# Optimization experiments

Measured on AMD Instinct MI355X. Metric: run time of the kernel, lower is better.

The kernel has to match this reference:

```python
import jax, jax.numpy as jnp
import numpy as np

B, C, H, W = 4, 64, 96, 96
KS, NH = 7, 4


def setup_inputs() -> dict:
    key = jax.random.key(0)
    ks = jax.random.split(key, 9)
    s = 0.1  # keep logits in a sane range for softmax
    return {
        "input_x": jax.random.normal(ks[0], (B, C, H, W), jnp.float32),
        "q_w": jax.random.normal(ks[1], (C, C), jnp.float32) * s,
        "q_b": jax.random.normal(ks[2], (C,), jnp.float32) * s,
        "k_w": jax.random.normal(ks[3], (C, C), jnp.float32) * s,
        "k_b": jax.random.normal(ks[4], (C,), jnp.float32) * s,
        "v_w": jax.random.normal(ks[5], (C, C), jnp.float32) * s,
        "v_b": jax.random.normal(ks[6], (C,), jnp.float32) * s,
        "rel_h": jax.random.normal(ks[7], (C // 2, KS, 1), jnp.float32) * s,
        "rel_w": jax.random.normal(ks[8], (C // 2, 1, KS), jnp.float32) * s,
    }


def _unfold(x, ks):
    # x: (B, C, Hp, Wp) -> (B, C, Ho, Wo, ks, ks), same as torch .unfold(2).unfold(3)
    Hp, Wp = x.shape[2], x.shape[3]
    Ho, Wo = Hp - ks + 1, Wp - ks + 1
    ih = jnp.arange(Ho)[:, None] + jnp.arange(ks)[None, :]  # (Ho, ks)
    iw = jnp.arange(Wo)[:, None] + jnp.arange(ks)[None, :]  # (Wo, ks)
    return x[:, :, ih[:, None, :, None], iw[None, :, None, :]]


def reference(input_x, q_w, q_b, k_w, k_b, v_w, v_b, rel_h, rel_w):
    b, c, h, w = input_x.shape
    ks, nh = KS, NH
    dkh = c // nh
    p0 = (ks - 1) // 2
    p1 = ks - 1 - p0
    padded = jnp.pad(input_x, ((0, 0), (0, 0), (p0, p1), (p0, p1)))

    conv1x1 = lambda x, wt, bi: jnp.einsum('bchw,oc->bohw', x, wt) + bi[None, :, None, None]
    k = conv1x1(padded, k_w, k_b)
    v = conv1x1(padded, v_w, v_b)
    q = conv1x1(input_x, q_w, q_b)

    # flat reshapes exactly as in torch (row-major), reproducing its layout semantics
    k = _unfold(k, ks).reshape(b, nh, h, w, dkh, ks * ks)
    v = _unfold(v, ks).reshape(b, nh, h, w, dkh, ks * ks)
    q = q.reshape(b, nh, h, w, dkh)  # torch: (b,nh,h,w,dkh,1) squeezed

    qk = jnp.einsum('bnxyd,bnxydk->bnxyk', q, k).reshape(b, nh, h, w, ks, ks)
    # torch einsum 'bhxydz,cij->bhxyij' == (sum_d q) outer (sum_c rel)
    qsum = q.sum(-1)  # (b, nh, h, w)
    rel = rel_h.sum(0) + rel_w.sum(0)  # broadcasts to (ks, ks)
    qk = qk + qsum[..., None, None] * rel

    weights = jax.nn.softmax(qk.reshape(b, nh, h, w, ks * ks), axis=-1)
    attn = jnp.einsum('bnxyk,bnxydk->bnxyd', weights, v)  # (b, nh, h, w, dkh)
    attn = attn.reshape(b, c, h, w)  # flat reshape, matching torch
    return jax.nn.relu(attn)
```

## Files before the change

### kernel.cpp

```cpp
#include <hip/hip_runtime.h>

#define B_ 4
#define C_ 64
#define H_ 96
#define W_ 96
#define KS_ 7
#define NPIX (H_ * W_)
#define PR_ 102
#define PC_ 104
#define PSLAB (PR_ * PC_)

typedef __attribute__((ext_vector_type(8))) short short8;
typedef __attribute__((ext_vector_type(8))) unsigned short ushort8;
typedef __attribute__((ext_vector_type(4))) float f32x4;

static __device__ inline ushort f2bf(float f) {
    union { float f; unsigned u; } v; v.f = f;
    unsigned r = (v.u + 0x7fff + ((v.u >> 16) & 1)) >> 16;
    return (ushort)r;
}
static __device__ inline float bf2f(ushort u) {
    union { unsigned u; float f; } v; v.u = ((unsigned)u) << 16; return v.f;
}


__global__ __launch_bounds__(256) void mfma_conv_kernel(
    const float* __restrict__ in,
    const float* __restrict__ qw, const float* __restrict__ qb,
    const float* __restrict__ kw, const float* __restrict__ kb,
    const float* __restrict__ vw, const float* __restrict__ vb,
    const float* __restrict__ relh, const float* __restrict__ relw,
    float* __restrict__ qf, ushort* __restrict__ kvb, float* __restrict__ rel_out)
{
    const int b    = blockIdx.y;
    const int pix0 = blockIdx.x * 32;
    const int t    = threadIdx.x;
    const int lane = t & 63;
    const int wv   = t >> 6;

    if (blockIdx.x == 0 && b == 0 && t < 49) {
        const int i = t / KS_, j = t % KS_;
        float s = 0.f;
        #pragma unroll
        for (int cc = 0; cc < C_ / 2; ++cc)
            s += relh[cc * KS_ + i] + relw[cc * KS_ + j];
        rel_out[t] = s;
    }

    {
        const int base = blockIdx.x * 256 + t;
        #pragma unroll
        for (int rep = 0; rep < 3; ++rep) {
            const int idx = base + rep * 73728;
            if (idx < 153600) {
                const int cell   = idx % 1200;
                const int chh    = (idx / 1200) & 63;
                const int tensor = idx / 76800;
                int pr, pw;
                if (cell < 312)      { pr = cell / PC_;              pw = cell % PC_; }
                else if (cell < 624) { int j2 = cell - 312; pr = 99 + j2 / PC_; pw = j2 % PC_; }
                else                 { int j2 = cell - 624; pr = 3 + j2 / 6; int s2 = j2 % 6;
                                       pw = (s2 < 3) ? s2 : 96 + s2; }
                const float bias = (tensor ? vb : kb)[chh];
                kvb[((size_t)(b * 2 + tensor) * C_ + chh) * PSLAB + pr * PC_ + pw] = f2bf(bias);
            }
        }
    }

    __shared__ ushort xs[32 * 64];

    {
        const int pix = t & 31, cg = t >> 5;
        const float* xp = in + (size_t)b * C_ * NPIX + pix0 + pix;
        #pragma unroll
        for (int g = 0; g < 2; ++g) {
            const int ch = (cg + 8 * g) * 4;
            float x0 = xp[(size_t)(ch    ) * NPIX];
            float x1 = xp[(size_t)(ch + 1) * NPIX];
            float x2 = xp[(size_t)(ch + 2) * NPIX];
            float x3 = xp[(size_t)(ch + 3) * NPIX];
            ushort4 u = make_ushort4(f2bf(x0), f2bf(x1), f2bf(x2), f2bf(x3));
            unsigned byte = (unsigned)(pix * 128 + ch * 2) ^ (unsigned)((pix & 7) << 4);
            *reinterpret_cast<ushort4*>(reinterpret_cast<char*>(xs) + byte) = u;
        }
    }

    short8 afr[3][2];
    float  bi[3][4];
    #pragma unroll
    for (int i = 0; i < 3; ++i) {
        const int mt  = 3 * wv + i;
        const int row = mt * 16 + (lane & 15);
        const float* wsrc = (mt < 4) ? qw + row * 64
                          : (mt < 8) ? kw + (row - 64) * 64
                                     : vw + (row - 128) * 64;
        #pragma unroll
        for (int ka = 0; ka < 2; ++ka) {
            const int kk = ka * 32 + (lane >> 4) * 8;
            float4 a = *reinterpret_cast<const float4*>(wsrc + kk);
            float4 c = *reinterpret_cast<const float4*>(wsrc + kk + 4);
            short8 s;
            s[0] = (short)f2bf(a.x); s[1] = (short)f2bf(a.y);
            s[2] = (short)f2bf(a.z); s[3] = (short)f2bf(a.w);
            s[4] = (short)f2bf(c.x); s[5] = (short)f2bf(c.y);
            s[6] = (short)f2bf(c.z); s[7] = (short)f2bf(c.w);
            afr[i][ka] = s;
        }
        const int brow = mt * 16 + (lane >> 4) * 4;
        const float* bsrc = (mt < 4) ? qb + brow
                          : (mt < 8) ? kb + (brow - 64)
                                     : vb + (brow - 128);
        #pragma unroll
        for (int r = 0; r < 4; ++r) bi[i][r] = bsrc[r];
    }
    __syncthreads();

    short8 bfr[2][2];
    #pragma unroll
    for (int nt = 0; nt < 2; ++nt) {
        const int pl = nt * 16 + (lane & 15);
        #pragma unroll
        for (int ka = 0; ka < 2; ++ka) {
            const int kk = ka * 32 + (lane >> 4) * 8;
            unsigned byte = (unsigned)(pl * 128 + kk * 2) ^ (unsigned)((pl & 7) << 4);
            bfr[nt][ka] = *reinterpret_cast<const short8*>(
                reinterpret_cast<const char*>(xs) + byte);
        }
    }
    f32x4 acc[3][2];
    #pragma unroll
    for (int i = 0; i < 3; ++i) {
        f32x4 bv;
        #pragma unroll
        for (int r = 0; r < 4; ++r) bv[r] = bi[i][r];
        #pragma unroll
        for (int nt = 0; nt < 2; ++nt) acc[i][nt] = bv;
    }
    #pragma unroll
    for (int i = 0; i < 3; ++i) {
        #pragma unroll
        for (int nt = 0; nt < 2; ++nt) {
            acc[i][nt] = __builtin_amdgcn_mfma_f32_16x16x32_bf16(
                afr[i][0], bfr[nt][0], acc[i][nt], 0, 0, 0);
            acc[i][nt] = __builtin_amdgcn_mfma_f32_16x16x32_bf16(
                afr[i][1], bfr[nt][1], acc[i][nt], 0, 0, 0);
        }
    }
    #pragma unroll
    for (int i = 0; i < 3; ++i) {
        const int mt = 3 * wv + i;
        #pragma unroll
        for (int nt = 0; nt < 2; ++nt) {
            const int pix = pix0 + nt * 16 + (lane & 15);
            const int h = pix / 96, w = pix - h * 96;
            #pragma unroll
            for (int r = 0; r < 4; ++r) {
                const int row = mt * 16 + (lane >> 4) * 4 + r;
                if (mt < 4) {
                    qf[((size_t)b * C_ + row) * NPIX + pix] = acc[i][nt][r];
                } else {
                    const int tensor = (mt < 8) ? 0 : 1;
                    const int ch = (mt & 3) * 16 + (lane >> 4) * 4 + r;
                    kvb[((size_t)(b * 2 + tensor) * C_ + ch) * PSLAB
                        + (h + 3) * PC_ + (w + 3)] = f2bf(acc[i][nt][r]);
                }
            }
        }
    }
}

__global__ __launch_bounds__(384) void attn_kernel(
    const float* __restrict__ qf, const ushort* __restrict__ kvb,
    const float* __restrict__ rel, float* __restrict__ out)
{
    const int bx   = blockIdx.x;
    const int tile = bx % 3;
    const int c    = (bx / 3) % C_;
    const int b    = bx / (3 * C_);
    const int ho0  = tile * 32;
    const int t    = threadIdx.x;

    __shared__ __align__(16) ushort kvls[2][38 * PC_];

    {
        const ushort* kbase = kvb + ((size_t)(b * 2 + 0) * C_ + c) * PSLAB + ho0 * PC_;
        const ushort* vbase = kvb + ((size_t)(b * 2 + 1) * C_ + c) * PSLAB + ho0 * PC_;
        #pragma unroll
        for (int s0 = 0; s0 < 3; ++s0) {
            const int idx = t + s0 * 384;
            if (idx < 988) {
                const int tensor = idx >= 494;
                const int off = (tensor ? idx - 494 : idx) * 8;
                const ushort* src = (tensor ? vbase : kbase) + off;
                *reinterpret_cast<ushort8*>(&kvls[tensor][off]) =
                    *reinterpret_cast<const ushort8*>(src);
            }
        }
    }
    __syncthreads();

    const int r0   = t / 12;
    const int rest = t % 12;
    const int w0   = (rest >> 1) * 16;
    const int half = rest & 1;
    const int ho   = ho0 + r0;

    const float LOG2E = 1.44269504f;
    const float* qp = qf + ((size_t)b * C_ + c) * NPIX + ho * W_ + w0;
    float qs[16];
    #pragma unroll
    for (int tt = 0; tt < 16; tt += 4) {
        float4 f = *reinterpret_cast<const float4*>(qp + tt);
        qs[tt] = f.x * LOG2E; qs[tt + 1] = f.y * LOG2E;
        qs[tt + 2] = f.z * LOG2E; qs[tt + 3] = f.w * LOG2E;
    }
    float qsum = 0.f;
    #pragma unroll
    for (int tt = 0; tt < 16; ++tt) qsum += qs[tt];

    float p[49];
    #pragma unroll
    for (int i = 0; i < KS_; ++i) {
        const ushort* kp = &kvls[0][(r0 + i) * PC_ + w0];
        ushort8 u0 = *reinterpret_cast<const ushort8*>(kp);
        ushort8 u1 = *reinterpret_cast<const ushort8*>(kp + 8);
        ushort8 u2 = *reinterpret_cast<const ushort8*>(kp + 16);
        float kr[22];
        #pragma unroll
        for (int e = 0; e < 8; ++e) kr[e] = bf2f(u0[e]);
        #pragma unroll
        for (int e = 0; e < 8; ++e) kr[8 + e] = bf2f(u1[e]);
        #pragma unroll
        for (int e = 0; e < 6; ++e) kr[16 + e] = bf2f(u2[e]);
        #pragma unroll
        for (int j = 0; j < KS_; ++j) {
            float s0 = 0.f, s1 = 0.f, s2 = 0.f, s3 = 0.f;
            #pragma unroll
            for (int tt = 0; tt < 16; tt += 4) {
                s0 = fmaf(qs[tt],     kr[tt + j],     s0);
                s1 = fmaf(qs[tt + 1], kr[tt + 1 + j], s1);
                s2 = fmaf(qs[tt + 2], kr[tt + 2 + j], s2);
                s3 = fmaf(qs[tt + 3], kr[tt + 3 + j], s3);
            }
            p[i * KS_ + j] = (s0 + s1) + (s2 + s3) + qsum * rel[i * KS_ + j];
        }
    }

    float m0 = p[0], m1 = p[1], m2 = p[2], m3 = p[3];
    #pragma unroll
    for (int kk = 4; kk < 48; kk += 4) {
        m0 = fmaxf(m0, p[kk]);     m1 = fmaxf(m1, p[kk + 1]);
        m2 = fmaxf(m2, p[kk + 2]); m3 = fmaxf(m3, p[kk + 3]);
    }
    float m = fmaxf(fmaxf(fmaxf(m0, m1), fmaxf(m2, m3)), p[48]);

    float e0 = 0.f, e1 = 0.f, e2 = 0.f, e3 = 0.f;
    #pragma unroll
    for (int kk = 0; kk < 48; kk += 4) {
        float a0 = exp2f(p[kk]     - m);
        float a1 = exp2f(p[kk + 1] - m);
        float a2 = exp2f(p[kk + 2] - m);
        float a3 = exp2f(p[kk + 3] - m);
        p[kk] = a0; p[kk + 1] = a1; p[kk + 2] = a2; p[kk + 3] = a3;
        e0 += a0; e1 += a1; e2 += a2; e3 += a3;
    }
    float a48 = exp2f(p[48] - m);
    p[48] = a48;
    const float inv = 1.f / ((e0 + e1) + (e2 + e3) + a48);

    float o8[8];
    #pragma unroll
    for (int d = 0; d < 8; ++d) o8[d] = 0.f;

    #pragma unroll
    for (int i = 0; i < KS_; ++i) {
        const ushort* vp = &kvls[1][(r0 + i) * PC_ + w0 + half * 8];
        ushort8 u0 = *reinterpret_cast<const ushort8*>(vp);
        ushort8 u1 = *reinterpret_cast<const ushort8*>(vp + 8);
        float vf[14];
        #pragma unroll
        for (int e = 0; e < 8; ++e) vf[e] = bf2f(u0[e]);
        #pragma unroll
        for (int e = 0; e < 6; ++e) vf[8 + e] = bf2f(u1[e]);
        #pragma unroll
        for (int j = 0; j < KS_; ++j) {
            float wgt = p[i * KS_ + j];
            #pragma unroll
            for (int d = 0; d < 8; ++d) o8[d] = fmaf(wgt, vf[d + j], o8[d]);
        }
    }

    float* op = out + (((size_t)b * C_ + c) * H_ + ho) * W_ + w0 + half * 8;
    #pragma unroll
    for (int d = 0; d < 8; d += 4) {
        float4 f;
        f.x = fmaxf(o8[d]     * inv, 0.f);
        f.y = fmaxf(o8[d + 1] * inv, 0.f);
        f.z = fmaxf(o8[d + 2] * inv, 0.f);
        f.w = fmaxf(o8[d + 3] * inv, 0.f);
        *reinterpret_cast<float4*>(op + d) = f;
    }
}

extern "C" void kernel_launch(void* const* d_in, const int* in_sizes, int n_in,
                              void* d_out, int out_size, void* d_ws, size_t ws_size,
                              hipStream_t stream) {
    const float* in   = (const float*)d_in[0];
    const float* qw   = (const float*)d_in[1];
    const float* qb   = (const float*)d_in[2];
    const float* kw   = (const float*)d_in[3];
    const float* kb   = (const float*)d_in[4];
    const float* vw   = (const float*)d_in[5];
    const float* vb   = (const float*)d_in[6];
    const float* relh = (const float*)d_in[7];
    const float* relw = (const float*)d_in[8];
    float* out = (float*)d_out;

    float*  qf  = (float*)d_ws;
    ushort* kvb = (ushort*)(qf + (size_t)B_ * C_ * NPIX);
    float*  rel = (float*)(kvb + (size_t)B_ * 2 * C_ * PSLAB);

    dim3 cgrid(NPIX / 32, B_);
    mfma_conv_kernel<<<cgrid, 256, 0, stream>>>(in, qw, qb, kw, kb, vw, vb,
                                                relh, relw, qf, kvb, rel);

    dim3 agrid(B_ * C_ * 3);
    attn_kernel<<<agrid, 384, 0, stream>>>(qf, kvb, rel, out);
}
```

Baseline: 40.15 us.

## Store K/V intermediates in fp32 and give each attention thread 16 outputs

The conv kernel now writes the padded K and V slabs as fp32 instead of bf16. The attention kernel stages them in padded fp32 shared-memory tiles with row stride 108, which drops the bf16 unpack work. Block size is halved to 192 threads, and each thread now computes all 16 output pixels instead of splitting V accumulation across two threads, so the recomputed QK/softmax work is no longer duplicated. The cost is twice the global traffic and footprint for the K/V workspace and more registers per thread, which may lower occupancy.

```diff
diff --git a/kernel.cpp b/kernel.cpp
--- a/kernel.cpp
+++ b/kernel.cpp
@@ -9,18 +9,15 @@
 #define PR_ 102
 #define PC_ 104
 #define PSLAB (PR_ * PC_)
+#define LDK 108
 
 typedef __attribute__((ext_vector_type(8))) short short8;
-typedef __attribute__((ext_vector_type(8))) unsigned short ushort8;
 typedef __attribute__((ext_vector_type(4))) float f32x4;
 
 static __device__ inline ushort f2bf(float f) {
     union { float f; unsigned u; } v; v.f = f;
     unsigned r = (v.u + 0x7fff + ((v.u >> 16) & 1)) >> 16;
     return (ushort)r;
-}
-static __device__ inline float bf2f(ushort u) {
-    union { unsigned u; float f; } v; v.u = ((unsigned)u) << 16; return v.f;
 }
 
 
@@ -30,7 +27,7 @@
     const float* __restrict__ kw, const float* __restrict__ kb,
     const float* __restrict__ vw, const float* __restrict__ vb,
     const float* __restrict__ relh, const float* __restrict__ relw,
-    float* __restrict__ qf, ushort* __restrict__ kvb, float* __restrict__ rel_out)
+    float* __restrict__ qf, float* __restrict__ kvf, float* __restrict__ rel_out)
 {
     const int b    = blockIdx.y;
     const int pix0 = blockIdx.x * 32;
@@ -62,7 +59,7 @@
                 else                 { int j2 = cell - 624; pr = 3 + j2 / 6; int s2 = j2 % 6;
                                        pw = (s2 < 3) ? s2 : 96 + s2; }
                 const float bias = (tensor ? vb : kb)[chh];
-                kvb[((size_t)(b * 2 + tensor) * C_ + chh) * PSLAB + pr * PC_ + pw] = f2bf(bias);
+                kvf[((size_t)(b * 2 + tensor) * C_ + chh) * PSLAB + pr * PC_ + pw] = bias;
             }
         }
     }
@@ -161,16 +158,16 @@
                 } else {
                     const int tensor = (mt < 8) ? 0 : 1;
                     const int ch = (mt & 3) * 16 + (lane >> 4) * 4 + r;
-                    kvb[((size_t)(b * 2 + tensor) * C_ + ch) * PSLAB
-                        + (h + 3) * PC_ + (w + 3)] = f2bf(acc[i][nt][r]);
+                    kvf[((size_t)(b * 2 + tensor) * C_ + ch) * PSLAB
+                        + (h + 3) * PC_ + (w + 3)] = acc[i][nt][r];
                 }
             }
         }
     }
 }
 
-__global__ __launch_bounds__(384) void attn_kernel(
-    const float* __restrict__ qf, const ushort* __restrict__ kvb,
+__global__ __launch_bounds__(192) void attn_kernel(
+    const float* __restrict__ qf, const float* __restrict__ kvf,
     const float* __restrict__ rel, float* __restrict__ out)
 {
     const int bx   = blockIdx.x;
@@ -180,30 +177,29 @@
     const int ho0  = tile * 32;
     const int t    = threadIdx.x;
 
-    __shared__ __align__(16) ushort kvls[2][38 * PC_];
+    __shared__ __align__(16) float ksl[38 * LDK];
+    __shared__ __align__(16) float vsl[38 * LDK];
 
     {
-        const ushort* kbase = kvb + ((size_t)(b * 2 + 0) * C_ + c) * PSLAB + ho0 * PC_;
-        const ushort* vbase = kvb + ((size_t)(b * 2 + 1) * C_ + c) * PSLAB + ho0 * PC_;
-        #pragma unroll
-        for (int s0 = 0; s0 < 3; ++s0) {
-            const int idx = t + s0 * 384;
+        const float* kbase = kvf + ((size_t)(b * 2 + 0) * C_ + c) * PSLAB + ho0 * PC_;
+        const float* vbase = kvf + ((size_t)(b * 2 + 1) * C_ + c) * PSLAB + ho0 * PC_;
+        #pragma unroll
+        for (int s0 = 0; s0 < 6; ++s0) {
+            const int idx = t + s0 * 192;
             if (idx < 988) {
-                const int tensor = idx >= 494;
-                const int off = (tensor ? idx - 494 : idx) * 8;
-                const ushort* src = (tensor ? vbase : kbase) + off;
-                *reinterpret_cast<ushort8*>(&kvls[tensor][off]) =
-                    *reinterpret_cast<const ushort8*>(src);
+                const int rl = idx / 26, c4 = (idx - rl * 26) * 4;
+                *reinterpret_cast<float4*>(&ksl[rl * LDK + c4]) =
+                    *reinterpret_cast<const float4*>(kbase + rl * PC_ + c4);
+                *reinterpret_cast<float4*>(&vsl[rl * LDK + c4]) =
+                    *reinterpret_cast<const float4*>(vbase + rl * PC_ + c4);
             }
         }
     }
     __syncthreads();
 
-    const int r0   = t / 12;
-    const int rest = t % 12;
-    const int w0   = (rest >> 1) * 16;
-    const int half = rest & 1;
-    const int ho   = ho0 + r0;
+    const int r0 = t / 6;
+    const int w0 = (t % 6) * 16;
+    const int ho = ho0 + r0;
 
     const float LOG2E = 1.44269504f;
     const float* qp = qf + ((size_t)b * C_ + c) * NPIX + ho * W_ + w0;
@@ -221,17 +217,13 @@
     float p[49];
     #pragma unroll
     for (int i = 0; i < KS_; ++i) {
-        const ushort* kp = &kvls[0][(r0 + i) * PC_ + w0];
-        ushort8 u0 = *reinterpret_cast<const ushort8*>(kp);
-        ushort8 u1 = *reinterpret_cast<const ushort8*>(kp + 8);
-        ushort8 u2 = *reinterpret_cast<const ushort8*>(kp + 16);
-        float kr[22];
-        #pragma unroll
-        for (int e = 0; e < 8; ++e) kr[e] = bf2f(u0[e]);
-        #pragma unroll
-        for (int e = 0; e < 8; ++e) kr[8 + e] = bf2f(u1[e]);
-        #pragma unroll
-        for (int e = 0; e < 6; ++e) kr[16 + e] = bf2f(u2[e]);
+        float kr[24];
+        const float* kp = &ksl[(r0 + i) * LDK + w0];
+        #pragma unroll
+        for (int tt = 0; tt < 24; tt += 4) {
+            float4 f = *reinterpret_cast<const float4*>(kp + tt);
+            kr[tt] = f.x; kr[tt + 1] = f.y; kr[tt + 2] = f.z; kr[tt + 3] = f.w;
+        }
         #pragma unroll
         for (int j = 0; j < KS_; ++j) {
             float s0 = 0.f, s1 = 0.f, s2 = 0.f, s3 = 0.f;
@@ -268,36 +260,35 @@
     p[48] = a48;
     const float inv = 1.f / ((e0 + e1) + (e2 + e3) + a48);
 
-    float o8[8];
-    #pragma unroll
-    for (int d = 0; d < 8; ++d) o8[d] = 0.f;
+    float o16[16];
+    #pragma unroll
+    for (int d = 0; d < 16; ++d) o16[d] = 0.f;
 
     #pragma unroll
     for (int i = 0; i < KS_; ++i) {
-        const ushort* vp = &kvls[1][(r0 + i) * PC_ + w0 + half * 8];
-        ushort8 u0 = *reinterpret_cast<const ushort8*>(vp);
-        ushort8 u1 = *reinterpret_cast<const ushort8*>(vp + 8);
-        float vf[14];
-        #pragma unroll
-        for (int e = 0; e < 8; ++e) vf[e] = bf2f(u0[e]);
-        #pragma unroll
-        for (int e = 0; e < 6; ++e) vf[8 + e] = bf2f(u1[e]);
+        float vf[24];
+        const float* vp = &vsl[(r0 + i) * LDK + w0];
+        #pragma unroll
+        for (int tt = 0; tt < 24; tt += 4) {
+            float4 f = *reinterpret_cast<const float4*>(vp + tt);
+            vf[tt] = f.x; vf[tt + 1] = f.y; vf[tt + 2] = f.z; vf[tt + 3] = f.w;
+        }
         #pragma unroll
         for (int j = 0; j < KS_; ++j) {
             float wgt = p[i * KS_ + j];
             #pragma unroll
-            for (int d = 0; d < 8; ++d) o8[d] = fmaf(wgt, vf[d + j], o8[d]);
-        }
-    }
-
-    float* op = out + (((size_t)b * C_ + c) * H_ + ho) * W_ + w0 + half * 8;
-    #pragma unroll
-    for (int d = 0; d < 8; d += 4) {
+            for (int d = 0; d < 16; ++d) o16[d] = fmaf(wgt, vf[d + j], o16[d]);
+        }
+    }
+
+    float* op = out + (((size_t)b * C_ + c) * H_ + ho) * W_ + w0;
+    #pragma unroll
+    for (int d = 0; d < 16; d += 4) {
         float4 f;
-        f.x = fmaxf(o8[d]     * inv, 0.f);
-        f.y = fmaxf(o8[d + 1] * inv, 0.f);
-        f.z = fmaxf(o8[d + 2] * inv, 0.f);
-        f.w = fmaxf(o8[d + 3] * inv, 0.f);
+        f.x = fmaxf(o16[d]     * inv, 0.f);
+        f.y = fmaxf(o16[d + 1] * inv, 0.f);
+        f.z = fmaxf(o16[d + 2] * inv, 0.f);
+        f.w = fmaxf(o16[d + 3] * inv, 0.f);
         *reinterpret_cast<float4*>(op + d) = f;
     }
 }
@@ -316,14 +307,14 @@
     const float* relw = (const float*)d_in[8];
     float* out = (float*)d_out;
 
-    float*  qf  = (float*)d_ws;
-    ushort* kvb = (ushort*)(qf + (size_t)B_ * C_ * NPIX);
-    float*  rel = (float*)(kvb + (size_t)B_ * 2 * C_ * PSLAB);
+    float* qf  = (float*)d_ws;
+    float* kvf = qf + (size_t)B_ * C_ * NPIX;
+    float* rel = kvf + (size_t)B_ * 2 * C_ * PSLAB;
 
     dim3 cgrid(NPIX / 32, B_);
     mfma_conv_kernel<<<cgrid, 256, 0, stream>>>(in, qw, qb, kw, kb, vw, vb,
-                                                relh, relw, qf, kvb, rel);
+                                                relh, relw, qf, kvf, rel);
 
     dim3 agrid(B_ * C_ * 3);
-    attn_kernel<<<agrid, 384, 0, stream>>>(qf, kvb, rel, out);
+    attn_kernel<<<agrid, 192, 0, stream>>>(qf, kvf, rel, out);
 }
```

Result: faster. 37.64 us (-6.2%).
